# Kernel tuning notes

Hardware: AMD Instinct MI355X
Metric: run time of the kernel (lower is better)

Reference implementation:

```python
import jax, jax.numpy as jnp
import numpy as np

NB, M, FIN = 8, 32768, 32       # batch, mesh vertices, input features
RANK, FILT = 5, 32              # Chebyshev order, output filters
E = 262144                      # nnz of rescaled Laplacian (~8 per row)


def setup_inputs() -> dict:
    key = jax.random.key(0)
    ks = jax.random.split(key, 6)
    x = jax.random.normal(ks[0], (NB, M, FIN), dtype=jnp.float32)
    rows = jax.random.randint(ks[1], (E,), 0, M, dtype=jnp.int32)
    cols = jax.random.randint(ks[2], (E,), 0, M, dtype=jnp.int32)
    # rescaled-Laplacian values, roughly spectral-normalized
    vals = jax.random.normal(ks[3], (E,), dtype=jnp.float32) * np.float32(1.0 / np.sqrt(8.0))
    kernel = jax.random.normal(ks[4], (FIN * RANK, FILT), dtype=jnp.float32) * np.float32(0.05)
    bias = jnp.zeros((FILT,), dtype=jnp.float32)
    return {"x": x, "vals": vals, "kernel": kernel, "bias": bias, "rows": rows, "cols": cols}


def _spmm(rows, cols, vals, x0):
    # y[m, f, n] = sum_j L[m, j] * x0[j, f, n]   (COO SpMM via gather + segment_sum)
    g = vals[:, None, None] * x0[cols]           # [E, Fin, N]
    return jax.ops.segment_sum(g, rows, num_segments=x0.shape[0])


def reference(x, vals, kernel, bias, rows, cols):
    N, Mm, Fin = x.shape
    x0 = jnp.transpose(x, (1, 2, 0))             # [M, Fin, N]
    xs = [x0]
    x1 = x0
    if RANK > 1:
        x1 = _spmm(rows, cols, vals, x0)         # T_1 = L x
        xs.append(x1)
    for _ in range(2, RANK):                     # T_k = 2 L T_{k-1} - T_{k-2}
        x2 = 2.0 * _spmm(rows, cols, vals, x1) - x0
        xs.append(x2)
        x0, x1 = x1, x2
    xk = jnp.stack(xs, axis=0)                   # [K, M, Fin, N]
    xk = jnp.transpose(xk, (3, 1, 2, 0)).reshape(N * Mm, Fin * RANK)  # Fin-major, rank inner
    out = xk @ kernel + bias                     # [N*M, FILT]
    return out.reshape(N, Mm, FILT)
```

## Files before the change

### kernel.cpp

```cpp
#include <hip/hip_runtime.h>

#define M_VERT 32768
#define NBATCH 8
#define FIN 32
#define RANK 5
#define FILT 32
#define E_NNZ 262144
#define ROWLEN 256
#define EPAD (E_NNZ + 15 * M_VERT)

typedef short short8 __attribute__((ext_vector_type(8)));
typedef float f32x4 __attribute__((ext_vector_type(4)));

__device__ __forceinline__ float bfl(unsigned int u) {
    unsigned int x = u << 16; return __builtin_bit_cast(float, x);
}
__device__ __forceinline__ float bfh(unsigned int u) {
    unsigned int x = u & 0xffff0000u; return __builtin_bit_cast(float, x);
}
__device__ __forceinline__ unsigned int f2bf(float f) {
    unsigned int x = __builtin_bit_cast(unsigned int, f);
    return (x + 0x7fffu + ((x >> 16) & 1u)) >> 16;
}
__device__ __forceinline__ unsigned int pk(float a, float b) {
    return f2bf(a) | (f2bf(b) << 16);
}


__global__ void pack_kernel(const float* __restrict__ x, unsigned short* __restrict__ T0,
                            const int* __restrict__ rows, int* __restrict__ cnt,
                            const float* __restrict__ W, unsigned short* __restrict__ Wb) {
    int tid = blockIdx.x * blockDim.x + threadIdx.x;
    int m = tid >> 5;
    int r = tid & 31;
    int n = r >> 2;
    int q = r & 3;
    const float* src = x + ((size_t)n * M_VERT + m) * FIN + q * 8;
    float4 v0 = *(const float4*)(src);
    float4 v1 = *(const float4*)(src + 4);
    uint4 u;
    u.x = pk(v0.x, v0.y); u.y = pk(v0.z, v0.w);
    u.z = pk(v1.x, v1.y); u.w = pk(v1.z, v1.w);
    *(uint4*)(T0 + (size_t)m * ROWLEN + n * FIN + q * 8) = u;

    if (tid < E_NNZ) atomicAdd(&cnt[rows[tid]], 1);

    if (tid < 640) {
        int lane = tid & 63;
        int kf = tid >> 6;
        int k = kf >> 1, ft = kf & 1;
        int f = ft * 16 + (lane & 15);
        int fin0 = (lane >> 4) * 8;
        unsigned short tmp[8];
#pragma unroll
        for (int j = 0; j < 8; ++j)
            tmp[j] = (unsigned short)f2bf(W[((fin0 + j) * RANK + k) * FILT + f]);
        uint4 uw;
        uw.x = (unsigned int)tmp[0] | ((unsigned int)tmp[1] << 16);
        uw.y = (unsigned int)tmp[2] | ((unsigned int)tmp[3] << 16);
        uw.z = (unsigned int)tmp[4] | ((unsigned int)tmp[5] << 16);
        uw.w = (unsigned int)tmp[6] | ((unsigned int)tmp[7] << 16);
        *(uint4*)(Wb + (size_t)tid * 8) = uw;
    }
}


__global__ __launch_bounds__(1024) void scan_kernel(const int* __restrict__ cnt,
                                                    int* __restrict__ rp,
                                                    int* __restrict__ fill) {
    __shared__ int sums[1024];
    int t = threadIdx.x;
    int base = t * 32;
    int local[32];
    int s = 0;
#pragma unroll
    for (int i = 0; i < 32; ++i) {
        int c = (cnt[base + i] + 15) & ~15;
        local[i] = c; s += c;
    }
    sums[t] = s;
    __syncthreads();
    for (int off = 1; off < 1024; off <<= 1) {
        int add = (t >= off) ? sums[t - off] : 0;
        __syncthreads();
        sums[t] += add;
        __syncthreads();
    }
    int pre = (t == 0) ? 0 : sums[t - 1];
#pragma unroll
    for (int i = 0; i < 32; ++i) { rp[base + i] = pre; pre += local[i]; }
    if (t == 1023) rp[M_VERT] = pre;
#pragma unroll
    for (int i = 0; i < 32; ++i) fill[base + i] = 0;
}

__global__ void scatter_kernel(const int* __restrict__ rows, const int* __restrict__ cols,
                               const float* __restrict__ vals, const int* __restrict__ rp,
                               int* __restrict__ fill, int2* __restrict__ ev) {
    int e = blockIdx.x * blockDim.x + threadIdx.x;
    if (e < E_NNZ) {
        int r = rows[e];
        int pos = rp[r] + atomicAdd(&fill[r], 1);
        int2 p; p.x = cols[e]; p.y = __builtin_bit_cast(int, vals[e]);
        ev[pos] = p;
    }
}


__global__ __launch_bounds__(256) void spmm_kernel(const int* __restrict__ rp,
                                                   const unsigned long long* __restrict__ ev,
                                                   const unsigned short* __restrict__ Tin,
                                                   const unsigned short* __restrict__ Tsub,
                                                   unsigned short* __restrict__ Tout, int cheb) {
    int w = threadIdx.x >> 6;
    int l = threadIdx.x & 63;
    int m = blockIdx.x * 4 + w;
    unsigned int coff = (unsigned int)l * 8u;
    int s = __builtin_amdgcn_readfirstlane(rp[m]);
    int e = __builtin_amdgcn_readfirstlane(rp[m + 1]);
    const char* tb = (const char*)Tin;
    float a0 = 0.f, a1 = 0.f, a2 = 0.f, a3 = 0.f;
    for (int j = s; j < e; j += 16) {
        unsigned long long ed[16];
#pragma unroll
        for (int i = 0; i < 16; ++i) ed[i] = ev[j + i];
        uint2 t[16];
#pragma unroll
        for (int i = 0; i < 16; ++i)
            t[i] = *(const uint2*)(tb + (((unsigned int)ed[i]) << 9) + coff);
#pragma unroll
        for (int i = 0; i < 16; ++i) {
            float v = __builtin_bit_cast(float, (unsigned int)(ed[i] >> 32));
            a0 += v * bfl(t[i].x); a1 += v * bfh(t[i].x);
            a2 += v * bfl(t[i].y); a3 += v * bfh(t[i].y);
        }
    }
    size_t moff = (size_t)m * 512 + coff;
    if (cheb) {
        unsigned long long o = __builtin_nontemporal_load(
            (const unsigned long long*)((const char*)Tsub + moff));
        unsigned int ox = (unsigned int)o, oy = (unsigned int)(o >> 32);
        a0 = 2.f * a0 - bfl(ox); a1 = 2.f * a1 - bfh(ox);
        a2 = 2.f * a2 - bfl(oy); a3 = 2.f * a3 - bfh(oy);
    }
    uint2 r;
    r.x = pk(a0, a1); r.y = pk(a2, a3);
    *(uint2*)((char*)Tout + moff) = r;
}


__global__ __launch_bounds__(256) void gemm_kernel(const unsigned short* __restrict__ T0,
                                                   const unsigned short* __restrict__ T1,
                                                   const unsigned short* __restrict__ T2,
                                                   const unsigned short* __restrict__ T3,
                                                   const unsigned short* __restrict__ T4,
                                                   const unsigned short* __restrict__ Wb,
                                                   const float* __restrict__ bias,
                                                   float* __restrict__ out) {
    int w = threadIdx.x >> 6;
    int l = threadIdx.x & 63;
    int n  = blockIdx.x & 7;
    int mb = blockIdx.x >> 3;
    int m0 = (mb * 4 + w) * 16;
    int lrow = l & 15;
    int quad = l >> 4;

    short8 bfrag[5][2];
#pragma unroll
    for (int kf = 0; kf < 10; ++kf)
        bfrag[kf >> 1][kf & 1] = *(const short8*)(Wb + ((size_t)kf * 64 + l) * 8);

    float b0 = bias[lrow];
    float b1 = bias[16 + lrow];

    const unsigned short* Ts[5] = {T0, T1, T2, T3, T4};
    size_t abase = (size_t)(m0 + lrow) * ROWLEN + quad * 8 + n * FIN;

    f32x4 c0 = {0.f, 0.f, 0.f, 0.f};
    f32x4 c1 = {0.f, 0.f, 0.f, 0.f};
#pragma unroll
    for (int k = 0; k < 5; ++k) {
        short8 a = *(const short8*)(Ts[k] + abase);
        c0 = __builtin_amdgcn_mfma_f32_16x16x32_bf16(a, bfrag[k][0], c0, 0, 0, 0);
        c1 = __builtin_amdgcn_mfma_f32_16x16x32_bf16(a, bfrag[k][1], c1, 0, 0, 0);
    }
    float* op = out + ((size_t)n * M_VERT + m0) * FILT;
#pragma unroll
    for (int r = 0; r < 4; ++r) {
        int orow = quad * 4 + r;
        __builtin_nontemporal_store(c0[r] + b0, &op[(size_t)orow * FILT + lrow]);
        __builtin_nontemporal_store(c1[r] + b1, &op[(size_t)orow * FILT + 16 + lrow]);
    }
}


extern "C" void kernel_launch(void* const* d_in, const int* in_sizes, int n_in,
                              void* d_out, int out_size, void* d_ws, size_t ws_size,
                              hipStream_t stream) {
    const float* x    = (const float*)d_in[0];
    const float* vals = (const float*)d_in[1];
    const float* W    = (const float*)d_in[2];
    const float* bias = (const float*)d_in[3];
    const int*   rows = (const int*)d_in[4];
    const int*   cols = (const int*)d_in[5];
    float* out = (float*)d_out;

    const size_t TSZ = (size_t)M_VERT * ROWLEN;
    unsigned short* T0 = (unsigned short*)d_ws;
    unsigned short* T1 = T0 + TSZ;
    unsigned short* T2 = T1 + TSZ;
    unsigned short* T3 = T2 + TSZ;
    unsigned short* T4 = T3 + TSZ;
    int*  rp   = (int*)(T4 + TSZ);
    int*  fill = rp + (M_VERT + 2);
    int2* ev   = (int2*)(fill + M_VERT);
    unsigned short* Wb = (unsigned short*)(ev + EPAD);

    hipMemsetAsync(fill, 0, M_VERT * sizeof(int), stream);
    hipMemsetAsync(ev, 0, (size_t)EPAD * sizeof(int2), stream);
    pack_kernel<<<M_VERT * 32 / 256, 256, 0, stream>>>(x, T0, rows, fill, W, Wb);
    scan_kernel<<<1, 1024, 0, stream>>>(fill, rp, fill);
    scatter_kernel<<<E_NNZ / 256, 256, 0, stream>>>(rows, cols, vals, rp, fill, ev);

    const unsigned long long* evq = (const unsigned long long*)ev;
    spmm_kernel<<<M_VERT / 4, 256, 0, stream>>>(rp, evq, T0, T0, T1, 0);
    spmm_kernel<<<M_VERT / 4, 256, 0, stream>>>(rp, evq, T1, T0, T2, 1);
    spmm_kernel<<<M_VERT / 4, 256, 0, stream>>>(rp, evq, T2, T1, T3, 1);
    spmm_kernel<<<M_VERT / 4, 256, 0, stream>>>(rp, evq, T3, T2, T4, 1);

    gemm_kernel<<<(M_VERT / 64) * 8, 256, 0, stream>>>(T0, T1, T2, T3, T4, Wb, bias, out);
}
```

Measured before the change: 263.4 us.

## Switch Chebyshev buffers to batch-major layout and split SpMM across batch

Stores each T_k as [batch][vertex][32] bf16 instead of vertex-major rows holding all batches. The SpMM launch is split per batch: a wave handles one row for one batch, with 8 lanes per edge over 8 edges at once, followed by a cross-lane shuffle reduction. Row padding drops from 16 to 8 edges. The aim is a smaller working set per batch slice so gathered rows hit in cache more often, at the cost of reading the edge list 8 times and adding the shuffle reductions.

Result: slower. 448.5 us (+70.3%).

```diff
diff --git a/kernel.cpp b/kernel.cpp
--- a/kernel.cpp
+++ b/kernel.cpp
@@ -7,7 +7,7 @@
 #define FILT 32
 #define E_NNZ 262144
 #define ROWLEN 256
-#define EPAD (E_NNZ + 15 * M_VERT)
+#define EPAD (E_NNZ + 7 * M_VERT)
 
 typedef short short8 __attribute__((ext_vector_type(8)));
 typedef float f32x4 __attribute__((ext_vector_type(4)));
@@ -31,17 +31,16 @@
                             const int* __restrict__ rows, int* __restrict__ cnt,
                             const float* __restrict__ W, unsigned short* __restrict__ Wb) {
     int tid = blockIdx.x * blockDim.x + threadIdx.x;
-    int m = tid >> 5;
-    int r = tid & 31;
-    int n = r >> 2;
-    int q = r & 3;
+    int q = tid & 3;
+    int m = (tid >> 2) & (M_VERT - 1);
+    int n = tid >> 17;
     const float* src = x + ((size_t)n * M_VERT + m) * FIN + q * 8;
     float4 v0 = *(const float4*)(src);
     float4 v1 = *(const float4*)(src + 4);
     uint4 u;
     u.x = pk(v0.x, v0.y); u.y = pk(v0.z, v0.w);
     u.z = pk(v1.x, v1.y); u.w = pk(v1.z, v1.w);
-    *(uint4*)(T0 + (size_t)m * ROWLEN + n * FIN + q * 8) = u;
+    *(uint4*)(T0 + ((size_t)n * M_VERT + m) * 32 + q * 8) = u;
 
     if (tid < E_NNZ) atomicAdd(&cnt[rows[tid]], 1);
 
@@ -75,7 +74,7 @@
     int s = 0;
 #pragma unroll
     for (int i = 0; i < 32; ++i) {
-        int c = (cnt[base + i] + 15) & ~15;
+        int c = (cnt[base + i] + 7) & ~7;
         local[i] = c; s += c;
     }
     sums[t] = s;
@@ -112,40 +111,46 @@
                                                    const unsigned short* __restrict__ Tin,
                                                    const unsigned short* __restrict__ Tsub,
                                                    unsigned short* __restrict__ Tout, int cheb) {
-    int w = threadIdx.x >> 6;
-    int l = threadIdx.x & 63;
-    int m = blockIdx.x * 4 + w;
-    unsigned int coff = (unsigned int)l * 8u;
+    int n  = blockIdx.x & 7;
+    int vb = blockIdx.x >> 3;
+    int w  = threadIdx.x >> 6;
+    int l  = threadIdx.x & 63;
+    int i  = l >> 3;
+    int k  = l & 7;
+    int m  = vb * 4 + w;
     int s = __builtin_amdgcn_readfirstlane(rp[m]);
     int e = __builtin_amdgcn_readfirstlane(rp[m + 1]);
-    const char* tb = (const char*)Tin;
+    const char* sb = (const char*)Tin + ((size_t)n << 21);
+    unsigned int kof = (unsigned int)k * 8u;
     float a0 = 0.f, a1 = 0.f, a2 = 0.f, a3 = 0.f;
-    for (int j = s; j < e; j += 16) {
-        unsigned long long ed[16];
-#pragma unroll
-        for (int i = 0; i < 16; ++i) ed[i] = ev[j + i];
-        uint2 t[16];
-#pragma unroll
-        for (int i = 0; i < 16; ++i)
-            t[i] = *(const uint2*)(tb + (((unsigned int)ed[i]) << 9) + coff);
-#pragma unroll
-        for (int i = 0; i < 16; ++i) {
-            float v = __builtin_bit_cast(float, (unsigned int)(ed[i] >> 32));
-            a0 += v * bfl(t[i].x); a1 += v * bfh(t[i].x);
-            a2 += v * bfl(t[i].y); a3 += v * bfh(t[i].y);
+    for (int j = s; j < e; j += 8) {
+        unsigned long long ed = ev[j + i];
+        unsigned int col = (unsigned int)ed;
+        float v = __builtin_bit_cast(float, (unsigned int)(ed >> 32));
+        uint2 t = *(const uint2*)(sb + (col << 6) + kof);
+        a0 += v * bfl(t.x); a1 += v * bfh(t.x);
+        a2 += v * bfl(t.y); a3 += v * bfh(t.y);
+    }
+#pragma unroll
+    for (int off = 8; off <= 32; off <<= 1) {
+        a0 += __shfl_xor(a0, off);
+        a1 += __shfl_xor(a1, off);
+        a2 += __shfl_xor(a2, off);
+        a3 += __shfl_xor(a3, off);
+    }
+    if (l < 8) {
+        size_t moff = ((size_t)n << 21) + ((size_t)((unsigned int)m << 6) + kof);
+        if (cheb) {
+            unsigned long long o = __builtin_nontemporal_load(
+                (const unsigned long long*)((const char*)Tsub + moff));
+            unsigned int ox = (unsigned int)o, oy = (unsigned int)(o >> 32);
+            a0 = 2.f * a0 - bfl(ox); a1 = 2.f * a1 - bfh(ox);
+            a2 = 2.f * a2 - bfl(oy); a3 = 2.f * a3 - bfh(oy);
         }
-    }
-    size_t moff = (size_t)m * 512 + coff;
-    if (cheb) {
-        unsigned long long o = __builtin_nontemporal_load(
-            (const unsigned long long*)((const char*)Tsub + moff));
-        unsigned int ox = (unsigned int)o, oy = (unsigned int)(o >> 32);
-        a0 = 2.f * a0 - bfl(ox); a1 = 2.f * a1 - bfh(ox);
-        a2 = 2.f * a2 - bfl(oy); a3 = 2.f * a3 - bfh(oy);
-    }
-    uint2 r;
-    r.x = pk(a0, a1); r.y = pk(a2, a3);
-    *(uint2*)((char*)Tout + moff) = r;
+        unsigned long long r = (unsigned long long)pk(a0, a1)
+                             | ((unsigned long long)pk(a2, a3) << 32);
+        __builtin_nontemporal_store(r, (unsigned long long*)((char*)Tout + moff));
+    }
 }
 
 
@@ -174,7 +179,7 @@
     float b1 = bias[16 + lrow];
 
     const unsigned short* Ts[5] = {T0, T1, T2, T3, T4};
-    size_t abase = (size_t)(m0 + lrow) * ROWLEN + quad * 8 + n * FIN;
+    size_t abase = ((size_t)n * M_VERT + (m0 + lrow)) * 32 + quad * 8;
 
     f32x4 c0 = {0.f, 0.f, 0.f, 0.f};
     f32x4 c1 = {0.f, 0.f, 0.f, 0.f};
@@ -223,10 +228,10 @@
     scatter_kernel<<<E_NNZ / 256, 256, 0, stream>>>(rows, cols, vals, rp, fill, ev);
 
     const unsigned long long* evq = (const unsigned long long*)ev;
-    spmm_kernel<<<M_VERT / 4, 256, 0, stream>>>(rp, evq, T0, T0, T1, 0);
-    spmm_kernel<<<M_VERT / 4, 256, 0, stream>>>(rp, evq, T1, T0, T2, 1);
-    spmm_kernel<<<M_VERT / 4, 256, 0, stream>>>(rp, evq, T2, T1, T3, 1);
-    spmm_kernel<<<M_VERT / 4, 256, 0, stream>>>(rp, evq, T3, T2, T4, 1);
+    spmm_kernel<<<(M_VERT / 4) * 8, 256, 0, stream>>>(rp, evq, T0, T0, T1, 0);
+    spmm_kernel<<<(M_VERT / 4) * 8, 256, 0, stream>>>(rp, evq, T1, T0, T2, 1);
+    spmm_kernel<<<(M_VERT / 4) * 8, 256, 0, stream>>>(rp, evq, T2, T1, T3, 1);
+    spmm_kernel<<<(M_VERT / 4) * 8, 256, 0, stream>>>(rp, evq, T3, T2, T4, 1);
 
     gemm_kernel<<<(M_VERT / 64) * 8, 256, 0, stream>>>(T0, T1, T2, T3, T4, Wb, bias, out);
 }
```
